# Kernel tuning notes

Measured on AMD Instinct MI355X. Metric: run time of the kernel, lower is better.

The kernel has to match this reference:

```python
import jax, jax.numpy as jnp
import numpy as np

V, WD, H, B, S, A = 50000, 300, 300, 64, 128, 8
H2 = 2 * H
NEG = -1e9


def _reverse_padded(x, lens):
    # reverse each sequence within its valid length; zeros elsewhere
    T = x.shape[1]
    idx = lens[:, None] - 1 - jnp.arange(T)[None, :]          # [B,T]
    valid = (idx >= 0)
    idx = jnp.clip(idx, 0, T - 1)
    return jnp.take_along_axis(x, idx[:, :, None], axis=1) * valid[:, :, None]


def _lstm_dir(x, lens, Wih, Whh, bih, bhh):
    # single-direction LSTM; emulates pack_padded: state frozen and output 0 past lens
    Bn, T, _ = x.shape
    Hn = Whh.shape[1]
    h0 = jnp.zeros((Bn, Hn), x.dtype)
    valid = (jnp.arange(T)[None, :] < lens[:, None]).astype(x.dtype)  # [B,T]

    def step(carry, inp):
        h, c = carry
        xt, vt = inp                                          # xt [B,D], vt [B,1]
        g = xt @ Wih.T + bih + h @ Whh.T + bhh                # [B,4H]
        i, f, gg, o = jnp.split(g, 4, axis=-1)                # torch gate order i,f,g,o
        i = jax.nn.sigmoid(i); f = jax.nn.sigmoid(f)
        o = jax.nn.sigmoid(o); gg = jnp.tanh(gg)
        c_new = f * c + i * gg
        h_new = o * jnp.tanh(c_new)
        h = vt * h_new + (1.0 - vt) * h
        c = vt * c_new + (1.0 - vt) * c
        return (h, c), vt * h_new

    _, outs = jax.lax.scan(step, (h0, h0), (x.transpose(1, 0, 2), valid.T[:, :, None]))
    return outs.transpose(1, 0, 2)                            # [B,T,H]


def _bilstm(x, lens, Wih, Whh, bih, bhh):
    fwd = _lstm_dir(x, lens, Wih[0], Whh[0], bih[0], bhh[0])
    xr = _reverse_padded(x, lens)
    bwd = _lstm_dir(xr, lens, Wih[1], Whh[1], bih[1], bhh[1])
    bwd = _reverse_padded(bwd, lens)
    return jnp.concatenate([fwd, bwd], axis=-1)               # [B,T,2H]


def setup_inputs() -> dict:
    key = jax.random.key(0)
    ks = jax.random.split(key, 16)
    lens_t = jax.random.randint(ks[0], (B,), S // 2, S + 1)
    ids_t = jax.random.randint(ks[1], (B, S), 1, V)
    text = jnp.where(jnp.arange(S)[None, :] < lens_t[:, None], ids_t, 0)
    lens_a = jax.random.randint(ks[2], (B,), 2, A + 1)
    ids_a = jax.random.randint(ks[3], (B, A), 1, V)
    aspect_ids = jnp.where(jnp.arange(A)[None, :] < lens_a[:, None], ids_a, 0)
    position_weight = jax.random.uniform(ks[4], (B, S), jnp.float32) * (text != 0)
    s = 0.05
    emb = jax.random.normal(ks[5], (V, WD), jnp.float32) * s
    emb = emb.at[0].set(0.0)  # padding row

    def lstm_params(k):
        k1, k2, k3, k4 = jax.random.split(k, 4)
        return (jax.random.normal(k1, (2, 4 * H, WD), jnp.float32) * s,
                jax.random.normal(k2, (2, 4 * H, H), jnp.float32) * s,
                jax.random.normal(k3, (2, 4 * H), jnp.float32) * s,
                jax.random.normal(k4, (2, 4 * H), jnp.float32) * s)

    l1_Wih, l1_Whh, l1_bih, l1_bhh = lstm_params(ks[6])
    l2_Wih, l2_Whh, l2_bih, l2_bhh = lstm_params(ks[7])
    return dict(
        text=text, aspect_ids=aspect_ids, position_weight=position_weight, emb=emb,
        l1_Wih=l1_Wih, l1_Whh=l1_Whh, l1_bih=l1_bih, l1_bhh=l1_bhh,
        l2_Wih=l2_Wih, l2_Whh=l2_Whh, l2_bih=l2_bih, l2_bhh=l2_bhh,
        lin1_W=jax.random.normal(ks[8], (2, H2, 2 * H2), jnp.float32) * s,
        lin1_b=jax.random.normal(ks[9], (2, H2), jnp.float32) * s,
        lin2_W=jax.random.normal(ks[10], (2, 1, H2), jnp.float32) * s,
        lin2_b=jax.random.normal(ks[11], (2, 1), jnp.float32) * s,
        fc_W=jax.random.normal(ks[12], (3, H2), jnp.float32) * s,
        fc_b=jax.random.normal(ks[13], (3,), jnp.float32) * s,
    )


def reference(text, aspect_ids, position_weight, emb,
              l1_Wih, l1_Whh, l1_bih, l1_bhh,
              l2_Wih, l2_Whh, l2_bih, l2_bhh,
              lin1_W, lin1_b, lin2_W, lin2_b, fc_W, fc_b):
    text_len = jnp.sum(text != 0, axis=-1)
    asp_len = jnp.sum(aspect_ids != 0, axis=-1)
    masks = (text != 0).astype(jnp.float32)          # [B,S]
    tmasks = (aspect_ids != 0).astype(jnp.float32)   # [B,A]
    wf = emb[text]                                    # [B,S,WD]
    af = emb[aspect_ids]                              # [B,A,WD]
    v = _bilstm(wf, text_len, l1_Wih, l1_Whh, l1_bih, l1_bhh)   # [B,S,2H]
    e = _bilstm(af, asp_len, l2_Wih, l2_Whh, l2_bih, l2_bhh)    # [B,A,2H]
    pair_mask = masks[:, :, None] * tmasks[:, None, :]          # [B,S,A]
    for i in range(2):
        a = jnp.einsum('bsd,bad->bsa', v, e)
        a = jnp.where(pair_mask == 0, NEG, a)
        a = jax.nn.softmax(a, axis=2)
        mid = jnp.einsum('bsa,bad->bsd', a, e)                  # [B,S,2H]
        mid = jnp.concatenate([mid, v], axis=-1)                # [B,S,4H]
        mid = jax.nn.leaky_relu(mid @ lin1_W[i].T + lin1_b[i])  # [B,S,2H]
        t = jax.nn.sigmoid(v @ lin2_W[i].T + lin2_b[i])         # [B,S,1]
        v = (1.0 - t) * mid + t * v
        v = position_weight[:, :, None] * v
    e_masked = jnp.where(tmasks[:, :, None] == 0, NEG, e)
    query = jnp.max(e_masked, axis=1)                           # [B,2H]
    alpha = jnp.einsum('bsd,bd->bs', v, query)
    alpha = jnp.where(masks == 0, NEG, alpha)
    alpha = jax.nn.softmax(alpha, axis=1)
    z = jnp.einsum('bs,bsd->bd', alpha, v)                      # [B,2H]
    return z @ fc_W.T + fc_b                                    # [B,3]
```

## Files before the change

### kernel.cpp

```cpp
#include <hip/hip_runtime.h>
#include <hip/hip_bf16.h>
#include <hip/hip_fp16.h>


typedef unsigned short u16;
typedef __attribute__((ext_vector_type(8))) short short8;
typedef __attribute__((ext_vector_type(4))) float floatx4;

#define NEGV -1e9f
#define MFMA __builtin_amdgcn_mfma_f32_16x16x32_bf16

__device__ __forceinline__ float bf2f(u16 u) {
    union { unsigned int i; float f; } x; x.i = ((unsigned int)u) << 16; return x.f;
}
__device__ __forceinline__ u16 f2bf(float f) {
    unsigned int u = __float_as_uint(f);
    unsigned int r = (u + 0x7fff + ((u >> 16) & 1)) >> 16;
    return (u16)r;
}
__device__ __forceinline__ float h16(u16 u) {
    __half h; *(u16*)&h = u; return __half2float(h);
}
__device__ __forceinline__ u16 f16(float f) {
    __half h = __float2half(f); return *(u16*)&h;
}
__device__ __forceinline__ float sigm(float x) { return 1.f / (1.f + expf(-x)); }
__device__ __forceinline__ float rdf(const void* p, size_t i, int flag) {
    return flag ? ((const float*)p)[i] : bf2f(((const u16*)p)[i]);
}

#if defined(__has_builtin)
# if __has_builtin(__builtin_amdgcn_fdot2)
#  define USE_FDOT2_BUILTIN 1
# endif
#endif
typedef __attribute__((ext_vector_type(2))) _Float16 half2v;
__device__ __forceinline__ float dot2f(unsigned int w, unsigned int h, float acc) {
#ifdef USE_FDOT2_BUILTIN
    union { unsigned int u; half2v v; } a, b;
    a.u = w; b.u = h;
    return __builtin_amdgcn_fdot2(a.v, b.v, acc, false);
#else
    asm("v_dot2_f32_f16 %0, %1, %2, %0" : "+v"(acc) : "v"(w), "v"(h));
    return acc;
#endif
}

__global__ void k_detect(const void* __restrict__ emb, int* __restrict__ flag) {
    __shared__ int cnt;
    if (threadIdx.x == 0) cnt = 0;
    __syncthreads();
    u16 x = ((const u16*)emb)[4096 + threadIdx.x];
    int e = (x >> 7) & 0xFF;
    if (e >= 0x8A) atomicAdd(&cnt, 1);
    __syncthreads();
    if (threadIdx.x == 0) *flag = (cnt > 8) ? 1 : 0;
}

__global__ void k_prep_small(const int* __restrict__ text, const int* __restrict__ asp,
                             int* __restrict__ lens) {
    int tid = threadIdx.x;
    if (tid < 64) {
        int c = 0;
        for (int s = 0; s < 128; ++s) c += (text[tid * 128 + s] != 0);
        lens[tid] = c;
    } else if (tid < 128) {
        int b = tid - 64; int c = 0;
        for (int a = 0; a < 8; ++a) c += (asp[b * 8 + a] != 0);
        lens[64 + b] = c;
    }
}

__global__ void k_pad_wih2(const void* __restrict__ W1, const void* __restrict__ W2,
                           const int* __restrict__ flag,
                           u16* __restrict__ d1h, u16* __restrict__ d1l,
                           u16* __restrict__ d2h, u16* __restrict__ d2l) {
    int i = blockIdx.x * 256 + threadIdx.x;
    if (i >= 2 * 2432 * 320) return;
    int f = *flag;
    int layer = i / (2432 * 320), r = i - layer * (2432 * 320);
    int n = r / 320, k = r - n * 320;
    const void* W = layer ? W2 : W1;
    float val = (n < 2400 && k < 300) ? rdf(W, (size_t)n * 300 + k, f) : 0.f;
    u16 hi = f2bf(val);
    float lo = val - bf2f(hi);
    if (layer) { d2h[r] = hi; d2l[r] = f2bf(lo); }
    else       { d1h[r] = hi; d1l[r] = f2bf(lo); }
}

__global__ void k_whhT2(const void* __restrict__ W1, const void* __restrict__ W2,
                        const int* __restrict__ flag,
                        u16* __restrict__ d1, u16* __restrict__ d2) {
    int i = blockIdx.x * 256 + threadIdx.x;
    if (i >= 2 * 720000) return;
    int f = *flag;
    int layer = i / 720000, r = i - layer * 720000;
    int dir = r / 360000, rr = r - dir * 360000;
    int kp = rr / 2400, t = rr - kp * 2400;
    int cc = t >> 1, j = t & 1;
    int k = 2 * kp + j;
    const void* W = layer ? W2 : W1;
    u16 bits = f16(rdf(W, (size_t)dir * 360000 + (size_t)cc * 300 + k, f));
    if (layer) d2[r] = bits; else d1[r] = bits;
}

__global__ void k_pad_lin1AB(const void* __restrict__ W, const int* __restrict__ flag,
                             u16* __restrict__ Ahi, u16* __restrict__ Alo,
                             u16* __restrict__ Bhi, u16* __restrict__ Blo) {
    int i = blockIdx.x * 256 + threadIdx.x;
    if (i >= 2 * 640 * 608) return;
    int f = *flag;
    int it = i / (640 * 608), r = i - it * (640 * 608);
    int n = r / 608, k = r - n * 608;
    float va = 0.f, vb = 0.f;
    if (n < 600 && k < 600) {
        va = rdf(W, (size_t)it * 720000 + (size_t)n * 1200 + k, f);
        vb = rdf(W, (size_t)it * 720000 + (size_t)n * 1200 + 600 + k, f);
    }
    u16 h;
    h = f2bf(va); Ahi[i] = h; Alo[i] = f2bf(va - bf2f(h));
    h = f2bf(vb); Bhi[i] = h; Blo[i] = f2bf(vb - bf2f(h));
}

__global__ void k_esplit(const float* __restrict__ e,
                         u16* __restrict__ ehi, u16* __restrict__ elo) {
    int i = blockIdx.x * 256 + threadIdx.x;
    if (i >= 512 * 608) return;
    int r = i / 608, k = i - r * 608;
    float val = (k < 600) ? e[r * 600 + k] : 0.f;
    u16 h = f2bf(val);
    ehi[i] = h;
    elo[i] = f2bf(val - bf2f(h));
}

__global__ void k_small(const void* pw, const void* l2w, const void* l2b,
                        const void* fcw, const void* fcb, const void* lb,
                        const void* b1i, const void* b1h, const void* b2i, const void* b2h,
                        const int* __restrict__ flag,
                        float* __restrict__ dst, float* __restrict__ bl,
                        float* __restrict__ bt, float* __restrict__ ba) {
    int i = blockIdx.x * 256 + threadIdx.x;
    int f = *flag;
    if (i < 8192)            dst[i] = rdf(pw, i, f);
    else if (i < 9392)       dst[i] = rdf(l2w, i - 8192, f);
    else if (i < 9394)       dst[i] = rdf(l2b, i - 9392, f);
    else if (i < 11194)      dst[i] = rdf(fcw, i - 9394, f);
    else if (i < 11197)      dst[i] = rdf(fcb, i - 11194, f);
    if (i < 1280) {
        int dir = i / 640, c = i - dir * 640;
        bl[i] = (c < 600) ? rdf(lb, dir * 600 + c, f) : 0.f;
    }
    if (i < 2400) {
        bt[i] = rdf(b1i, i, f) + rdf(b1h, i, f);
        ba[i] = rdf(b2i, i, f) + rdf(b2h, i, f);
    }
}

__device__ __forceinline__ void gemm_emb_tile(
    const void* __restrict__ emb, const int* __restrict__ ids,
    int base, int rpb, int stride, int f,
    const u16* __restrict__ Bhi, const u16* __restrict__ Blo,
    const float* __restrict__ bias,
    u16* __restrict__ C, int ldc, int nstore, int bx, int by, int tid)
{
    int wave = tid >> 6, lane = tid & 63;
    int l15 = lane & 15, quad = lane >> 4;
    int m0 = bx * 64 + wave * 16;
    int n0 = by * 64;

    int m = m0 + l15;
    int b = m / rpb, j = m - b * rpb;
    int id = ids[b * stride + base + j];
    const float* arow_f = (const float*)emb + (size_t)id * 300;
    const u16*   arow_b = (const u16*)emb + (size_t)id * 300;

    const u16* Bp  = Bhi + (size_t)(n0 + l15) * 320 + quad * 8;
    const u16* Bp2 = Blo + (size_t)(n0 + l15) * 320 + quad * 8;

    floatx4 acc0 = {0.f, 0.f, 0.f, 0.f};
    floatx4 acc1 = acc0, acc2 = acc0, acc3 = acc0;

    for (int kc = 0; kc < 10; ++kc) {
        int ko = kc * 32 + quad * 8;
        short8 ahi, alo;
        if (f) {
            if (ko + 8 <= 300) {
                float4 fa = *(const float4*)(arow_f + ko);
                float4 fb = *(const float4*)(arow_f + ko + 4);
                float vv[8] = {fa.x, fa.y, fa.z, fa.w, fb.x, fb.y, fb.z, fb.w};
                #pragma unroll
                for (int t = 0; t < 8; ++t) {
                    u16 h = f2bf(vv[t]);
                    ahi[t] = (short)h;
                    alo[t] = (short)f2bf(vv[t] - bf2f(h));
                }
            } else {
                #pragma unroll
                for (int t = 0; t < 8; ++t) {
                    int k = ko + t;
                    float vv = (k < 300) ? arow_f[k] : 0.f;
                    u16 h = f2bf(vv);
                    ahi[t] = (short)h;
                    alo[t] = (short)f2bf(vv - bf2f(h));
                }
            }
        } else {
            #pragma unroll
            for (int t = 0; t < 8; ++t) {
                int k = ko + t;
                ahi[t] = (k < 300) ? (short)arow_b[k] : (short)0;
                alo[t] = 0;
            }
        }
        int ko2 = kc * 32;
        short8 bh0 = *(const short8*)(Bp + ko2);
        short8 bh1 = *(const short8*)(Bp + (size_t)16 * 320 + ko2);
        short8 bh2 = *(const short8*)(Bp + (size_t)32 * 320 + ko2);
        short8 bh3 = *(const short8*)(Bp + (size_t)48 * 320 + ko2);
        short8 bl0 = *(const short8*)(Bp2 + ko2);
        short8 bl1 = *(const short8*)(Bp2 + (size_t)16 * 320 + ko2);
        short8 bl2 = *(const short8*)(Bp2 + (size_t)32 * 320 + ko2);
        short8 bl3 = *(const short8*)(Bp2 + (size_t)48 * 320 + ko2);
        acc0 = MFMA(ahi, bh0, acc0, 0, 0, 0);
        acc1 = MFMA(ahi, bh1, acc1, 0, 0, 0);
        acc2 = MFMA(ahi, bh2, acc2, 0, 0, 0);
        acc3 = MFMA(ahi, bh3, acc3, 0, 0, 0);
        acc0 = MFMA(ahi, bl0, acc0, 0, 0, 0);
        acc1 = MFMA(ahi, bl1, acc1, 0, 0, 0);
        acc2 = MFMA(ahi, bl2, acc2, 0, 0, 0);
        acc3 = MFMA(ahi, bl3, acc3, 0, 0, 0);
        acc0 = MFMA(alo, bh0, acc0, 0, 0, 0);
        acc1 = MFMA(alo, bh1, acc1, 0, 0, 0);
        acc2 = MFMA(alo, bh2, acc2, 0, 0, 0);
        acc3 = MFMA(alo, bh3, acc3, 0, 0, 0);
    }

    #pragma unroll
    for (int c = 0; c < 4; ++c) {
        floatx4 acc = (c == 0) ? acc0 : (c == 1) ? acc1 : (c == 2) ? acc2 : acc3;
        int col = n0 + c * 16 + l15;
        if (col >= nstore) continue;
        float bb = bias[col];
        #pragma unroll
        for (int r = 0; r < 4; ++r) {
            int row = m0 + quad * 4 + r;
            C[(size_t)row * ldc + col] = f16(acc[r] + bb);
        }
    }
}

__global__ __launch_bounds__(256) void gemm_embk(
    const void* __restrict__ emb, const int* __restrict__ ids,
    int base, int rpb, int stride, const int* __restrict__ flag,
    const u16* __restrict__ Bhi, const u16* __restrict__ Blo,
    const float* __restrict__ bias,
    u16* __restrict__ C, int ldc, int nstore)
{
    gemm_emb_tile(emb, ids, base, rpb, stride, *flag, Bhi, Blo, bias,
                  C, ldc, nstore, blockIdx.x, blockIdx.y, threadIdx.x);
}

__device__ __forceinline__ void gemm_core(
    const u16* __restrict__ Ap, const u16* __restrict__ Ap2,
    const u16* __restrict__ Bp, const u16* __restrict__ Bp2,
    int lda, int ldb, int nk,
    floatx4& acc0, floatx4& acc1, floatx4& acc2, floatx4& acc3)
{
    for (int kc = 0; kc < nk; ++kc) {
        int ko = kc * 32;
        short8 bh0 = *(const short8*)(Bp + ko);
        short8 bh1 = *(const short8*)(Bp + (size_t)16 * ldb + ko);
        short8 bh2 = *(const short8*)(Bp + (size_t)32 * ldb + ko);
        short8 bh3 = *(const short8*)(Bp + (size_t)48 * ldb + ko);
        short8 bl0 = *(const short8*)(Bp2 + ko);
        short8 bl1 = *(const short8*)(Bp2 + (size_t)16 * ldb + ko);
        short8 bl2 = *(const short8*)(Bp2 + (size_t)32 * ldb + ko);
        short8 bl3 = *(const short8*)(Bp2 + (size_t)48 * ldb + ko);
        short8 a  = *(const short8*)(Ap + ko);
        short8 al = *(const short8*)(Ap2 + ko);
        acc0 = MFMA(a, bh0, acc0, 0, 0, 0);
        acc1 = MFMA(a, bh1, acc1, 0, 0, 0);
        acc2 = MFMA(a, bh2, acc2, 0, 0, 0);
        acc3 = MFMA(a, bh3, acc3, 0, 0, 0);
        acc0 = MFMA(a, bl0, acc0, 0, 0, 0);
        acc1 = MFMA(a, bl1, acc1, 0, 0, 0);
        acc2 = MFMA(a, bl2, acc2, 0, 0, 0);
        acc3 = MFMA(a, bl3, acc3, 0, 0, 0);
        acc0 = MFMA(al, bh0, acc0, 0, 0, 0);
        acc1 = MFMA(al, bh1, acc1, 0, 0, 0);
        acc2 = MFMA(al, bh2, acc2, 0, 0, 0);
        acc3 = MFMA(al, bh3, acc3, 0, 0, 0);
    }
}

__global__ __launch_bounds__(256) void gemm_ew(
    const u16* __restrict__ Ahi, const u16* __restrict__ Alo,
    const u16* __restrict__ l1a_hi, const u16* __restrict__ l1a_lo,
    float* __restrict__ EW)
{
    int tid = threadIdx.x;
    int wave = tid >> 6, lane = tid & 63;
    int l15 = lane & 15, quad = lane >> 4;
    int iter = blockIdx.z;
    int m0 = blockIdx.x * 64 + wave * 16;
    int n0 = blockIdx.y * 64;
    const u16* Ap  = Ahi + (size_t)(m0 + l15) * 608 + quad * 8;
    const u16* Ap2 = Alo + (size_t)(m0 + l15) * 608 + quad * 8;
    const u16* Bp  = l1a_hi + (size_t)iter * 640 * 608 + (size_t)(n0 + l15) * 608 + quad * 8;
    const u16* Bp2 = l1a_lo + (size_t)iter * 640 * 608 + (size_t)(n0 + l15) * 608 + quad * 8;
    floatx4 acc0 = {0.f, 0.f, 0.f, 0.f};
    floatx4 acc1 = acc0, acc2 = acc0, acc3 = acc0;
    gemm_core(Ap, Ap2, Bp, Bp2, 608, 608, 19, acc0, acc1, acc2, acc3);
    #pragma unroll
    for (int c = 0; c < 4; ++c) {
        floatx4 acc = (c == 0) ? acc0 : (c == 1) ? acc1 : (c == 2) ? acc2 : acc3;
        int col = n0 + c * 16 + l15;
        if (col >= 600) continue;
        #pragma unroll
        for (int r = 0; r < 4; ++r) {
            int row = m0 + quad * 4 + r;
            EW[((size_t)iter * 512 + row) * 600 + col] = acc[r];
        }
    }
}

__global__ __launch_bounds__(256) void gemm_vt(
    const u16* __restrict__ vhi, const u16* __restrict__ vlo,
    const u16* __restrict__ Bhi, const u16* __restrict__ Blo,
    const float* __restrict__ bias,
    const float* __restrict__ EW, const float* __restrict__ a_sm,
    const float* __restrict__ tg, const float* __restrict__ pw,
    float* __restrict__ vio)
{
    __shared__ float al_s[64][8];
    __shared__ float ew_s[8][64];
    int tid = threadIdx.x;
    int wave = tid >> 6, lane = tid & 63;
    int l15 = lane & 15, quad = lane >> 4;
    int m0 = blockIdx.x * 64 + wave * 16;
    int n0 = blockIdx.y * 64;
    int row0 = blockIdx.x * 64;
    int bidx = row0 >> 7;

    for (int i = tid; i < 512; i += 256)
        al_s[i >> 3][i & 7] = a_sm[(size_t)(row0 + (i >> 3)) * 8 + (i & 7)];
    for (int i = tid; i < 512; i += 256) {
        int a = i >> 6, cc = i & 63;
        int col = n0 + cc;
        ew_s[a][cc] = (col < 600) ? EW[((size_t)bidx * 8 + a) * 600 + col] : 0.f;
    }
    __syncthreads();

    const u16* Ap  = vhi + (size_t)(m0 + l15) * 608 + quad * 8;
    const u16* Ap2 = vlo + (size_t)(m0 + l15) * 608 + quad * 8;
    const u16* Bp  = Bhi + (size_t)(n0 + l15) * 608 + quad * 8;
    const u16* Bp2 = Blo + (size_t)(n0 + l15) * 608 + quad * 8;
    floatx4 acc0 = {0.f, 0.f, 0.f, 0.f};
    floatx4 acc1 = acc0, acc2 = acc0, acc3 = acc0;
    gemm_core(Ap, Ap2, Bp, Bp2, 608, 608, 19, acc0, acc1, acc2, acc3);

    #pragma unroll
    for (int c = 0; c < 4; ++c) {
        floatx4 acc = (c == 0) ? acc0 : (c == 1) ? acc1 : (c == 2) ? acc2 : acc3;
        int cc = c * 16 + l15;
        int col = n0 + cc;
        if (col >= 600) continue;
        float bb = bias[col];
        #pragma unroll
        for (int r = 0; r < 4; ++r) {
            int rr = wave * 16 + quad * 4 + r;
            int row = row0 + rr;
            float mid = 0.f;
            #pragma unroll
            for (int a = 0; a < 8; ++a) mid += al_s[rr][a] * ew_s[a][cc];
            float val = acc[r] + bb + mid;
            val = val > 0.f ? val : 0.01f * val;
            float t = tg[row];
            size_t vi = (size_t)row * 600 + col;
            float vv = vio[vi];
            vio[vi] = pw[row] * ((1.f - t) * val + t * vv);
        }
    }
}

__global__ __launch_bounds__(960, 1) void k_lstm6(
    const u16* __restrict__ xf, const u16* __restrict__ xb, int ldx, int rpb,
    int base_f, int base_b, const u16* __restrict__ whhT,
    const int* __restrict__ lens, float* __restrict__ out, int T, int init,
    float* __restrict__ hst, float* __restrict__ cst, int nsteps,
    const u16* __restrict__ xa, const u16* __restrict__ whhA,
    const int* __restrict__ lensA, float* __restrict__ outA,
    float* __restrict__ hstA, float* __restrict__ cstA, int nLstm,
    const void* __restrict__ emb, const int* __restrict__ text,
    int bf_next, int bb_next, const int* __restrict__ flag,
    const u16* __restrict__ wih_hi, const u16* __restrict__ wih_lo,
    const float* __restrict__ bias_t,
    u16* __restrict__ xf_next, u16* __restrict__ xb_next)
{
    __shared__ float part2[6][2][600];
    __shared__ u16 wlds[6][4][2][1200];
    __shared__ __align__(4) u16 hs16[304];
    int blk = blockIdx.x;
    if (blk >= nLstm) {
        if (threadIdx.x >= 256) return;
        int g = blk - nLstm;
        int dirn = g / 608; int t = g - dirn * 608;
        int bx = t & 31, by = t >> 5;
        gemm_emb_tile(emb, text, dirn ? bb_next : bf_next, 32, 128, *flag,
                      wih_hi + (dirn ? 1200ull * 320 : 0),
                      wih_lo + (dirn ? 1200ull * 320 : 0),
                      bias_t + (dirn ? 1200 : 0),
                      dirn ? xb_next : xf_next, 1200, 1200, bx, by, threadIdx.x);
        return;
    }
    if (blk >= 128) {
        blk -= 128;
        xf = xa; xb = xa + 1200; ldx = 2400; rpb = 8;
        base_f = 0; base_b = 0;
        whhT = whhA; lens = lensA; out = outA; T = 8; init = 1;
        hst = hstA; cst = cstA; nsteps = 8;
    }
    int tid = threadIdx.x;
    int g6 = tid / 160, u = tid - g6 * 160;
    bool act = (u < 150);
    int b = blk >> 1, dir = blk & 1;
    int len = lens[b];
    float c = 0.f, hf = 0.f;
    const u16* wbase = whhT + (size_t)dir * 360000 + (size_t)g6 * 60000 + 16 * u;

    uint4 wA[8], wB[8];
    if (act) {
        #pragma unroll
        for (int r = 0; r < 8; ++r) {
            wA[r] = *(const uint4*)(wbase + (size_t)r * 2400);
            wB[r] = *(const uint4*)(wbase + (size_t)r * 2400 + 8);
        }
        #pragma unroll
        for (int r = 0; r < 4; ++r) {
            *(uint4*)&wlds[g6][r][0][8 * u] = *(const uint4*)(wbase + (size_t)(8 + r) * 2400);
            *(uint4*)&wlds[g6][r][1][8 * u] = *(const uint4*)(wbase + (size_t)(8 + r) * 2400 + 8);
        }
    } else {
        #pragma unroll
        for (int r = 0; r < 8; ++r) {
            wA[r] = uint4{0u, 0u, 0u, 0u};
            wB[r] = uint4{0u, 0u, 0u, 0u};
        }
    }
    #pragma unroll
    for (int r = 0; r < 8; ++r) {
        asm volatile("" : "+v"(wA[r].x), "+v"(wA[r].y), "+v"(wA[r].z), "+v"(wA[r].w));
        asm volatile("" : "+v"(wB[r].x), "+v"(wB[r].y), "+v"(wB[r].z), "+v"(wB[r].w));
    }
    if (tid < 300) {
        hf = init ? 0.f : hst[(size_t)blk * 300 + tid];
        c  = init ? 0.f : cst[(size_t)blk * 300 + tid];
        hs16[tid] = f16(hf);
    }
    __syncthreads();
    const u16* wstream = wbase + (size_t)12 * 2400;

    for (int s = 0; s < nsteps; ++s) {
        int pos = dir ? (base_b + nsteps - 1 - s) : (base_f + s);
        if (pos >= len) continue;
        if (act) {
            float a0 = 0.f, a1 = 0.f, a2 = 0.f, a3 = 0.f;
            float a4 = 0.f, a5 = 0.f, a6 = 0.f, a7 = 0.f;
            const unsigned int* h2p = (const unsigned int*)(hs16 + g6 * 50);
            #define DOT8(va, vb, hh)                                   \
                a0 = dot2f((va).x, hh, a0); a1 = dot2f((va).y, hh, a1);\
                a2 = dot2f((va).z, hh, a2); a3 = dot2f((va).w, hh, a3);\
                a4 = dot2f((vb).x, hh, a4); a5 = dot2f((vb).y, hh, a5);\
                a6 = dot2f((vb).z, hh, a6); a7 = dot2f((vb).w, hh, a7);
            #pragma unroll
            for (int r = 0; r < 8; ++r) {
                unsigned int h2 = h2p[r];
                DOT8(wA[r], wB[r], h2);
            }
            #pragma unroll
            for (int r = 0; r < 4; ++r) {
                unsigned int h2 = h2p[8 + r];
                uint4 va = *(const uint4*)&wlds[g6][r][0][8 * u];
                uint4 vb = *(const uint4*)&wlds[g6][r][1][8 * u];
                DOT8(va, vb, h2);
            }
            const u16* wp = wstream;
            #pragma unroll 4
            for (int i = 0; i < 13; ++i) {
                unsigned int h2 = h2p[12 + i];
                uint4 va = *(const uint4*)wp;
                uint4 vb = *(const uint4*)(wp + 8);
                wp += 2400;
                DOT8(va, vb, h2);
            }
            #undef DOT8
            float4 w0 = {a0, a1, a2, a3};
            float4 w1 = {a4, a5, a6, a7};
            *(float4*)&part2[g6][0][4 * u] = w0;
            *(float4*)&part2[g6][1][4 * u] = w1;
        }
        __syncthreads();
        if (tid < 300) {
            const u16* xr = dir ? (xb + (size_t)(b * rpb + pos - base_b) * ldx)
                                : (xf + (size_t)(b * rpb + pos - base_f) * ldx);
            float gi = h16(xr[tid]), gf = h16(xr[300 + tid]);
            float gg = h16(xr[600 + tid]), go = h16(xr[900 + tid]);
            #pragma unroll
            for (int g = 0; g < 6; ++g) {
                int c0 = tid,       i0 = ((c0 >> 3) << 2) | (c0 & 3);
                int c1 = 300 + tid, i1 = ((c1 >> 3) << 2) | (c1 & 3);
                int c2 = 600 + tid, i2 = ((c2 >> 3) << 2) | (c2 & 3);
                int c3 = 900 + tid, i3 = ((c3 >> 3) << 2) | (c3 & 3);
                gi += part2[g][(c0 >> 2) & 1][i0];
                gf += part2[g][(c1 >> 2) & 1][i1];
                gg += part2[g][(c2 >> 2) & 1][i2];
                go += part2[g][(c3 >> 2) & 1][i3];
            }
            gi = sigm(gi); gf = sigm(gf); gg = tanhf(gg); go = sigm(go);
            c = gf * c + gi * gg;
            float hn = go * tanhf(c);
            out[((size_t)b * T + pos) * 600 + dir * 300 + tid] = hn;
            hf = hn;
            hs16[tid] = f16(hn);
        }
        __syncthreads();
    }
    if (tid < 300) {
        hst[(size_t)blk * 300 + tid] = hf;
        cst[(size_t)blk * 300 + tid] = c;
    }
}

__global__ __launch_bounds__(128) void k_scorev(
    const float* __restrict__ v, const float* __restrict__ e,
    const int* __restrict__ text, const int* __restrict__ asp,
    const float* __restrict__ l2w, const float* __restrict__ l2b, int iter,
    float* __restrict__ a_sm, float* __restrict__ tg,
    u16* __restrict__ vhi, u16* __restrict__ vlo)
{
    __shared__ float vs[600];
    __shared__ float red[2][9];
    int row = blockIdx.x;
    int b = row >> 7;
    int t = threadIdx.x, wv = t >> 6, lane = t & 63;
    const float* vrow = v + (size_t)row * 600;
    const float* eb = e + (size_t)b * 4800;
    const float* w2 = l2w + iter * 600;

    for (int d = t; d < 600; d += 128) vs[d] = vrow[d];
    __syncthreads();

    float acc[9];
    #pragma unroll
    for (int j = 0; j < 9; ++j) acc[j] = 0.f;
    for (int d = t; d < 600; d += 128) {
        float vv = vs[d];
        #pragma unroll
        for (int a = 0; a < 8; ++a) acc[a] += vv * eb[a * 600 + d];
        acc[8] += vv * w2[d];
    }
    #pragma unroll
    for (int off = 32; off >= 1; off >>= 1) {
        #pragma unroll
        for (int j = 0; j < 9; ++j) acc[j] += __shfl_down(acc[j], off, 64);
    }
    if (lane == 0) {
        #pragma unroll
        for (int j = 0; j < 9; ++j) red[wv][j] = acc[j];
    }
    __syncthreads();
    if (t == 0) {
        float dots[9];
        #pragma unroll
        for (int j = 0; j < 9; ++j) dots[j] = red[0][j] + red[1][j];
        tg[row] = sigm(dots[8] + l2b[iter]);
        bool sm = (text[row] != 0);
        float sc[8]; float mx = -INFINITY;
        #pragma unroll
        for (int a = 0; a < 8; ++a) {
            sc[a] = (sm && asp[b * 8 + a] != 0) ? dots[a] : NEGV;
            mx = fmaxf(mx, sc[a]);
        }
        float den = 0.f;
        #pragma unroll
        for (int a = 0; a < 8; ++a) { sc[a] = expf(sc[a] - mx); den += sc[a]; }
        float inv = 1.f / den;
        #pragma unroll
        for (int a = 0; a < 8; ++a) a_sm[(size_t)row * 8 + a] = sc[a] * inv;
    }
    for (int d = t; d < 608; d += 128) {
        float val = (d < 600) ? vs[d] : 0.f;
        u16 h = f2bf(val);
        vhi[(size_t)row * 608 + d] = h;
        vlo[(size_t)row * 608 + d] = f2bf(val - bf2f(h));
    }
}

__global__ void k_query(const float* __restrict__ e, const int* __restrict__ asp,
                        float* __restrict__ q) {
    int i = blockIdx.x * 256 + threadIdx.x;
    if (i >= 64 * 600) return;
    int b = i / 600, d = i - b * 600;
    float m = NEGV;
    for (int a = 0; a < 8; ++a)
        if (asp[b * 8 + a] != 0) m = fmaxf(m, e[(size_t)b * 4800 + a * 600 + d]);
    q[i] = m;
}

__global__ __launch_bounds__(128) void k_final(
    const float* __restrict__ v, const float* __restrict__ q,
    const int* __restrict__ text, const float* __restrict__ fcW,
    const float* __restrict__ fcb, const int* __restrict__ flag, void* __restrict__ outv)
{
    __shared__ float red[128];
    __shared__ float al[128];
    __shared__ float zz[600];
    int b = blockIdx.x, s = threadIdx.x;
    const float* vrow = v + (size_t)(b * 128 + s) * 600;
    const float* qb = q + (size_t)b * 600;
    float sc = 0.f;
    for (int d = 0; d < 600; ++d) sc += vrow[d] * qb[d];
    if (text[b * 128 + s] == 0) sc = NEGV;
    red[s] = sc; __syncthreads();
    for (int off = 64; off >= 1; off >>= 1) {
        if (s < off) red[s] = fmaxf(red[s], red[s + off]);
        __syncthreads();
    }
    float mx = red[0]; __syncthreads();
    float ex = expf(sc - mx);
    red[s] = ex; __syncthreads();
    for (int off = 64; off >= 1; off >>= 1) {
        if (s < off) red[s] += red[s + off];
        __syncthreads();
    }
    float alpha = ex / red[0];
    al[s] = alpha; __syncthreads();
    for (int d = s; d < 600; d += 128) {
        float z = 0.f;
        for (int s2 = 0; s2 < 128; ++s2) z += al[s2] * v[(size_t)(b * 128 + s2) * 600 + d];
        zz[d] = z;
    }
    __syncthreads();
    if (s < 3) {
        float o = 0.f;
        for (int d = 0; d < 600; ++d) o += zz[d] * fcW[s * 600 + d];
        o += fcb[s];
        if (*flag) ((float*)outv)[b * 3 + s] = o;
        else       ((u16*)outv)[b * 3 + s] = f2bf(o);
    }
}

extern "C" void kernel_launch(void* const* d_in, const int* in_sizes, int n_in,
                              void* d_out, int out_size, void* d_ws, size_t ws_size,
                              hipStream_t stream) {
    const int*  text   = (const int*)d_in[0];
    const int*  asp    = (const int*)d_in[1];
    const void* pw     = d_in[2];
    const void* emb    = d_in[3];
    const void* l1_Wih = d_in[4];
    const void* l1_Whh = d_in[5];
    const void* l1_bih = d_in[6];
    const void* l1_bhh = d_in[7];
    const void* l2_Wih = d_in[8];
    const void* l2_Whh = d_in[9];
    const void* l2_bih = d_in[10];
    const void* l2_bhh = d_in[11];
    const void* lin1_W = d_in[12];
    const void* lin1_b = d_in[13];
    const void* lin2_W = d_in[14];
    const void* lin2_b = d_in[15];
    const void* fcW    = d_in[16];
    const void* fcb    = d_in[17];
    (void)ws_size; (void)n_in; (void)in_sizes; (void)out_size;

    char* w = (char*)d_ws;
    size_t off = 0;
    auto alloc = [&](size_t bytes) -> void* {
        void* p = w + off;
        off += (bytes + 255) & ~(size_t)255;
        return p;
    };
    int*   flag     = (int*)  alloc(4);
    int*   lens     = (int*)  alloc(128ull * 4);
    float* bias_t   = (float*)alloc(2400ull * 4);
    float* bias_a   = (float*)alloc(2400ull * 4);
    float* bias_l1  = (float*)alloc(1280ull * 4);
    float* smallf   = (float*)alloc(11197ull * 4);
    float* tg       = (float*)alloc(8192ull * 4);
    float* a_sm     = (float*)alloc(8192ull * 8 * 4);
    float* query    = (float*)alloc(64ull * 600 * 4);
    float* hst_t    = (float*)alloc(128ull * 300 * 4);
    float* cst_t    = (float*)alloc(128ull * 300 * 4);
    float* hst_a    = (float*)alloc(128ull * 300 * 4);
    float* cst_a    = (float*)alloc(128ull * 300 * 4);
    float* e        = (float*)alloc(512ull * 600 * 4);
    float* v        = (float*)alloc(8192ull * 600 * 4);
    float* pw_f     = smallf;
    float* l2w_f    = smallf + 8192;
    float* l2b_f    = smallf + 9392;
    float* fcW_f    = smallf + 9394;
    float* fcb_f    = smallf + 11194;
    size_t phase_off = off;
    u16*   wiht_hi  = (u16*)  alloc(2432ull * 320 * 2);
    u16*   wiht_lo  = (u16*)  alloc(2432ull * 320 * 2);
    u16*   wiha_hi  = (u16*)  alloc(2432ull * 320 * 2);
    u16*   wiha_lo  = (u16*)  alloc(2432ull * 320 * 2);
    u16*   whhT_t   = (u16*)  alloc(720000ull * 2);
    u16*   whhT_a   = (u16*)  alloc(720000ull * 2);
    u16*   xf0      = (u16*)  alloc(2048ull * 1200 * 2);
    u16*   xb0      = (u16*)  alloc(2048ull * 1200 * 2);
    u16*   xf1      = (u16*)  alloc(2048ull * 1200 * 2);
    u16*   xb1      = (u16*)  alloc(2048ull * 1200 * 2);
    u16*   xproj_a  = (u16*)  alloc(512ull * 2400 * 2);
    off = phase_off;
    u16*   l1a_hi   = (u16*)  alloc(2ull * 640 * 608 * 2);
    u16*   l1a_lo   = (u16*)  alloc(2ull * 640 * 608 * 2);
    u16*   l1b_hi   = (u16*)  alloc(2ull * 640 * 608 * 2);
    u16*   l1b_lo   = (u16*)  alloc(2ull * 640 * 608 * 2);
    u16*   ehi      = (u16*)  alloc(512ull * 608 * 2);
    u16*   elo      = (u16*)  alloc(512ull * 608 * 2);
    float* EW       = (float*)alloc(2ull * 512 * 600 * 4);
    u16*   vhi      = (u16*)  alloc(8192ull * 608 * 2);
    u16*   vlo      = (u16*)  alloc(8192ull * 608 * 2);

    hipMemsetAsync(v, 0, 8192ull * 600 * 4, stream);
    hipMemsetAsync(e, 0, 512ull * 600 * 4, stream);

    k_detect<<<1, 256, 0, stream>>>(emb, flag);
    k_prep_small<<<1, 128, 0, stream>>>(text, asp, lens);
    k_pad_wih2<<<(2 * 2432 * 320 + 255) / 256, 256, 0, stream>>>(
        l1_Wih, l2_Wih, flag, wiht_hi, wiht_lo, wiha_hi, wiha_lo);
    k_whhT2<<<(2 * 720000 + 255) / 256, 256, 0, stream>>>(
        l1_Whh, l2_Whh, flag, whhT_t, whhT_a);
    k_small<<<49, 256, 0, stream>>>(pw, lin2_W, lin2_b, fcW, fcb, lin1_b,
                                    l1_bih, l1_bhh, l2_bih, l2_bhh, flag,
                                    smallf, bias_l1, bias_t, bias_a);

    gemm_embk<<<dim3(8, 38), 256, 0, stream>>>(emb, asp, 0, 8, 8, flag,
        wiha_hi, wiha_lo, bias_a, xproj_a, 2400, 2400);
    gemm_embk<<<dim3(32, 19), 256, 0, stream>>>(emb, text, 0, 32, 128, flag,
        wiht_hi, wiht_lo, bias_t, xf0, 1200, 1200);
    gemm_embk<<<dim3(32, 19), 256, 0, stream>>>(emb, text, 96, 32, 128, flag,
        wiht_hi + 1200ull * 320, wiht_lo + 1200ull * 320, bias_t + 1200,
        xb0, 1200, 1200);

    for (int kk = 0; kk < 4; ++kk) {
        int bf = 32 * kk;
        int bb = 96 - 32 * kk;
        u16* xfc = (kk & 1) ? xf1 : xf0;
        u16* xbc = (kk & 1) ? xb1 : xb0;
        u16* xfn = (kk & 1) ? xf0 : xf1;
        u16* xbn = (kk & 1) ? xb0 : xb1;
        int nLstm = (kk == 0) ? 256 : 128;
        int haveNext = (kk < 3);
        int nblk = nLstm + (haveNext ? 1216 : 0);
        k_lstm6<<<nblk, 960, 0, stream>>>(xfc, xbc, 1200, 32, bf, bb,
            whhT_t, lens, v, 128, kk == 0 ? 1 : 0, hst_t, cst_t, 32,
            xproj_a, whhT_a, lens + 64, e, hst_a, cst_a, nLstm,
            emb, text, bf + 32, bb - 32, flag, wiht_hi, wiht_lo, bias_t,
            xfn, xbn);
    }

    k_pad_lin1AB<<<(2 * 640 * 608 + 255) / 256, 256, 0, stream>>>(
        lin1_W, flag, l1a_hi, l1a_lo, l1b_hi, l1b_lo);
    k_esplit<<<(512 * 608 + 255) / 256, 256, 0, stream>>>(e, ehi, elo);
    gemm_ew<<<dim3(8, 10, 2), 256, 0, stream>>>(ehi, elo, l1a_hi, l1a_lo, EW);

    for (int iter = 0; iter < 2; ++iter) {
        k_scorev<<<8192, 128, 0, stream>>>(v, e, text, asp, l2w_f, l2b_f,
            iter, a_sm, tg, vhi, vlo);
        gemm_vt<<<dim3(128, 10), 256, 0, stream>>>(vhi, vlo,
            l1b_hi + (size_t)iter * 640 * 608, l1b_lo + (size_t)iter * 640 * 608,
            bias_l1 + iter * 640, EW + (size_t)iter * 512 * 600,
            a_sm, tg, pw_f, v);
    }

    k_query<<<150, 256, 0, stream>>>(e, asp, query);
    k_final<<<64, 128, 0, stream>>>(v, query, text, fcW_f, fcb_f, flag, d_out);
}
```

Measured before the change: 1.116 ms.

## Split each LSTM recurrence across two blocks exchanging partial gates via global memory

Each LSTM chain (batch, direction) is now split across a pair of workgroups, each owning half of the hidden units (150), so the kernel launches twice as many recurrent blocks. Each block computes partial gate pre-activations for all 1200 gates from its half of h, publishes the peer's half through a global exchange buffer, and spins on a per-block step counter flag for the peer's contribution. This spreads the serial recurrence over more CUs and drops the register-resident weights, but adds a cross-block global-memory handshake on every timestep. It also relies on both blocks of a pair being co-resident, which is a deadlock risk.

```diff
diff --git a/kernel.cpp b/kernel.cpp
--- a/kernel.cpp
+++ b/kernel.cpp
@@ -390,20 +390,21 @@
     float* __restrict__ hst, float* __restrict__ cst, int nsteps,
     const u16* __restrict__ xa, const u16* __restrict__ whhA,
     const int* __restrict__ lensA, float* __restrict__ outA,
-    float* __restrict__ hstA, float* __restrict__ cstA, int nLstm,
+    float* __restrict__ hstA, float* __restrict__ cstA, int nSplit,
     const void* __restrict__ emb, const int* __restrict__ text,
     int bf_next, int bb_next, const int* __restrict__ flag,
     const u16* __restrict__ wih_hi, const u16* __restrict__ wih_lo,
     const float* __restrict__ bias_t,
-    u16* __restrict__ xf_next, u16* __restrict__ xb_next)
+    u16* __restrict__ xf_next, u16* __restrict__ xb_next,
+    float* __restrict__ exch, unsigned int* __restrict__ flags)
 {
-    __shared__ float part2[6][2][600];
-    __shared__ u16 wlds[6][4][2][1200];
-    __shared__ __align__(4) u16 hs16[304];
+    __shared__ float part2[5][2][600];
+    __shared__ u16 wlds[5][2][2][1200];
+    __shared__ __align__(4) u16 hs16[152];
     int blk = blockIdx.x;
-    if (blk >= nLstm) {
+    if (blk >= nSplit) {
         if (threadIdx.x >= 256) return;
-        int g = blk - nLstm;
+        int g = blk - nSplit;
         int dirn = g / 608; int t = g - dirn * 608;
         int bx = t & 31, by = t >> 5;
         gemm_emb_tile(emb, text, dirn ? bb_next : bf_next, 32, 128, *flag,
@@ -413,81 +414,97 @@
                       dirn ? xb_next : xf_next, 1200, 1200, bx, by, threadIdx.x);
         return;
     }
-    if (blk >= 128) {
-        blk -= 128;
+    int me = blk, peer = blk ^ 1;
+    int kseg = blk & 1;
+    int chain = blk >> 1;
+    if (chain >= 128) {
+        chain -= 128;
         xf = xa; xb = xa + 1200; ldx = 2400; rpb = 8;
         base_f = 0; base_b = 0;
         whhT = whhA; lens = lensA; out = outA; T = 8; init = 1;
         hst = hstA; cst = cstA; nsteps = 8;
     }
     int tid = threadIdx.x;
-    int g6 = tid / 160, u = tid - g6 * 160;
+    int g6 = tid / 192, u = tid - g6 * 192;
     bool act = (u < 150);
-    int b = blk >> 1, dir = blk & 1;
+    int b = chain >> 1, dir = chain & 1;
     int len = lens[b];
     float c = 0.f, hf = 0.f;
-    const u16* wbase = whhT + (size_t)dir * 360000 + (size_t)g6 * 60000 + 16 * u;
-
-    uint4 wA[8], wB[8];
+    const u16* wbase = whhT + (size_t)dir * 360000
+                     + (size_t)(kseg * 75 + g6 * 15) * 2400 + 16 * u;
     if (act) {
         #pragma unroll
-        for (int r = 0; r < 8; ++r) {
-            wA[r] = *(const uint4*)(wbase + (size_t)r * 2400);
-            wB[r] = *(const uint4*)(wbase + (size_t)r * 2400 + 8);
-        }
-        #pragma unroll
-        for (int r = 0; r < 4; ++r) {
-            *(uint4*)&wlds[g6][r][0][8 * u] = *(const uint4*)(wbase + (size_t)(8 + r) * 2400);
-            *(uint4*)&wlds[g6][r][1][8 * u] = *(const uint4*)(wbase + (size_t)(8 + r) * 2400 + 8);
-        }
-    } else {
-        #pragma unroll
-        for (int r = 0; r < 8; ++r) {
-            wA[r] = uint4{0u, 0u, 0u, 0u};
-            wB[r] = uint4{0u, 0u, 0u, 0u};
-        }
-    }
+        for (int r = 0; r < 2; ++r) {
+            *(uint4*)&wlds[g6][r][0][8 * u] = *(const uint4*)(wbase + (size_t)r * 2400);
+            *(uint4*)&wlds[g6][r][1][8 * u] = *(const uint4*)(wbase + (size_t)r * 2400 + 8);
+        }
+    }
+    int e_abs = kseg * 150 + tid;
+    if (tid < 150) {
+        hf = init ? 0.f : hst[(size_t)chain * 300 + e_abs];
+        c  = init ? 0.f : cst[(size_t)chain * 300 + e_abs];
+        hs16[tid] = f16(hf);
+    }
+    int gH[4], gI[4];
     #pragma unroll
-    for (int r = 0; r < 8; ++r) {
-        asm volatile("" : "+v"(wA[r].x), "+v"(wA[r].y), "+v"(wA[r].z), "+v"(wA[r].w));
-        asm volatile("" : "+v"(wB[r].x), "+v"(wB[r].y), "+v"(wB[r].z), "+v"(wB[r].w));
-    }
-    if (tid < 300) {
-        hf = init ? 0.f : hst[(size_t)blk * 300 + tid];
-        c  = init ? 0.f : cst[(size_t)blk * 300 + tid];
-        hs16[tid] = f16(hf);
+    for (int k = 0; k < 4; ++k) {
+        int ck = e_abs + 300 * k;
+        gH[k] = (ck >> 2) & 1;
+        gI[k] = ((ck >> 3) << 2) | (ck & 3);
+    }
+    int pH = 0, pI = 0;
+    if (tid < 600) {
+        int r = tid % 150, q = tid / 150;
+        int pc = (kseg ^ 1) * 150 + r + 300 * q;
+        pH = (pc >> 2) & 1;
+        pI = ((pc >> 3) << 2) | (pc & 3);
+    }
+    float* exme = exch + (size_t)me * 1200;
+    const float* expe = exch + (size_t)peer * 1200;
+    unsigned int* flg_me = flags + me * 16;
+    unsigned int* flg_pe = flags + peer * 16;
+    unsigned int cnt = 0;
+    if (!init) {
+        if (dir == 0) {
+            int e0 = len < base_f ? len : base_f;
+            cnt = (unsigned)e0;
+        } else {
+            int kk = base_f >> 5;
+            for (int j = 0; j < kk; ++j) {
+                int e0 = len - (96 - 32 * j);
+                e0 = e0 < 0 ? 0 : (e0 > 32 ? 32 : e0);
+                cnt += (unsigned)e0;
+            }
+        }
     }
     __syncthreads();
-    const u16* wstream = wbase + (size_t)12 * 2400;
+    const u16* wstream = wbase + (size_t)2 * 2400;
+    const unsigned int* h2p = (const unsigned int*)hs16 + g6 * 15;
 
     for (int s = 0; s < nsteps; ++s) {
         int pos = dir ? (base_b + nsteps - 1 - s) : (base_f + s);
         if (pos >= len) continue;
+        ++cnt;
+        int par = (int)(cnt & 1u);
         if (act) {
             float a0 = 0.f, a1 = 0.f, a2 = 0.f, a3 = 0.f;
             float a4 = 0.f, a5 = 0.f, a6 = 0.f, a7 = 0.f;
-            const unsigned int* h2p = (const unsigned int*)(hs16 + g6 * 50);
             #define DOT8(va, vb, hh)                                   \
                 a0 = dot2f((va).x, hh, a0); a1 = dot2f((va).y, hh, a1);\
                 a2 = dot2f((va).z, hh, a2); a3 = dot2f((va).w, hh, a3);\
                 a4 = dot2f((vb).x, hh, a4); a5 = dot2f((vb).y, hh, a5);\
                 a6 = dot2f((vb).z, hh, a6); a7 = dot2f((vb).w, hh, a7);
             #pragma unroll
-            for (int r = 0; r < 8; ++r) {
+            for (int r = 0; r < 2; ++r) {
                 unsigned int h2 = h2p[r];
-                DOT8(wA[r], wB[r], h2);
-            }
-            #pragma unroll
-            for (int r = 0; r < 4; ++r) {
-                unsigned int h2 = h2p[8 + r];
                 uint4 va = *(const uint4*)&wlds[g6][r][0][8 * u];
                 uint4 vb = *(const uint4*)&wlds[g6][r][1][8 * u];
                 DOT8(va, vb, h2);
             }
             const u16* wp = wstream;
-            #pragma unroll 4
+            #pragma unroll 13
             for (int i = 0; i < 13; ++i) {
-                unsigned int h2 = h2p[12 + i];
+                unsigned int h2 = h2p[2 + i];
                 uint4 va = *(const uint4*)wp;
                 uint4 vb = *(const uint4*)(wp + 8);
                 wp += 2400;
@@ -500,34 +517,61 @@
             *(float4*)&part2[g6][1][4 * u] = w1;
         }
         __syncthreads();
-        if (tid < 300) {
+        if (tid < 600) {
+            float s5 = part2[0][pH][pI] + part2[1][pH][pI] + part2[2][pH][pI]
+                     + part2[3][pH][pI] + part2[4][pH][pI];
+            __hip_atomic_store(exme + par * 600 + tid, s5,
+                               __ATOMIC_RELAXED, __HIP_MEMORY_SCOPE_AGENT);
+        }
+        asm volatile("s_waitcnt vmcnt(0)" ::: "memory");
+        __syncthreads();
+        if (tid == 0) {
+            __hip_atomic_store(flg_me, cnt, __ATOMIC_RELEASE,
+                               __HIP_MEMORY_SCOPE_AGENT);
+            while (__hip_atomic_load(flg_pe, __ATOMIC_ACQUIRE,
+                                     __HIP_MEMORY_SCOPE_AGENT) < cnt)
+                __builtin_amdgcn_s_sleep(2);
+        }
+        __syncthreads();
+        if (tid < 150) {
             const u16* xr = dir ? (xb + (size_t)(b * rpb + pos - base_b) * ldx)
                                 : (xf + (size_t)(b * rpb + pos - base_f) * ldx);
-            float gi = h16(xr[tid]), gf = h16(xr[300 + tid]);
-            float gg = h16(xr[600 + tid]), go = h16(xr[900 + tid]);
-            #pragma unroll
-            for (int g = 0; g < 6; ++g) {
-                int c0 = tid,       i0 = ((c0 >> 3) << 2) | (c0 & 3);
-                int c1 = 300 + tid, i1 = ((c1 >> 3) << 2) | (c1 & 3);
-                int c2 = 600 + tid, i2 = ((c2 >> 3) << 2) | (c2 & 3);
-                int c3 = 900 + tid, i3 = ((c3 >> 3) << 2) | (c3 & 3);
-                gi += part2[g][(c0 >> 2) & 1][i0];
-                gf += part2[g][(c1 >> 2) & 1][i1];
-                gg += part2[g][(c2 >> 2) & 1][i2];
-                go += part2[g][(c3 >> 2) & 1][i3];
-            }
+            float p0 = part2[0][gH[0]][gI[0]] + part2[1][gH[0]][gI[0]]
+                     + part2[2][gH[0]][gI[0]] + part2[3][gH[0]][gI[0]]
+                     + part2[4][gH[0]][gI[0]];
+            float p1 = part2[0][gH[1]][gI[1]] + part2[1][gH[1]][gI[1]]
+                     + part2[2][gH[1]][gI[1]] + part2[3][gH[1]][gI[1]]
+                     + part2[4][gH[1]][gI[1]];
+            float p2 = part2[0][gH[2]][gI[2]] + part2[1][gH[2]][gI[2]]
+                     + part2[2][gH[2]][gI[2]] + part2[3][gH[2]][gI[2]]
+                     + part2[4][gH[2]][gI[2]];
+            float p3 = part2[0][gH[3]][gI[3]] + part2[1][gH[3]][gI[3]]
+                     + part2[2][gH[3]][gI[3]] + part2[3][gH[3]][gI[3]]
+                     + part2[4][gH[3]][gI[3]];
+            float q0 = __hip_atomic_load(expe + par * 600 + tid,
+                                         __ATOMIC_RELAXED, __HIP_MEMORY_SCOPE_AGENT);
+            float q1 = __hip_atomic_load(expe + par * 600 + 150 + tid,
+                                         __ATOMIC_RELAXED, __HIP_MEMORY_SCOPE_AGENT);
+            float q2 = __hip_atomic_load(expe + par * 600 + 300 + tid,
+                                         __ATOMIC_RELAXED, __HIP_MEMORY_SCOPE_AGENT);
+            float q3 = __hip_atomic_load(expe + par * 600 + 450 + tid,
+                                         __ATOMIC_RELAXED, __HIP_MEMORY_SCOPE_AGENT);
+            float gi = h16(xr[e_abs])       + p0 + q0;
+            float gf = h16(xr[300 + e_abs]) + p1 + q1;
+            float gg = h16(xr[600 + e_abs]) + p2 + q2;
+            float go = h16(xr[900 + e_abs]) + p3 + q3;
             gi = sigm(gi); gf = sigm(gf); gg = tanhf(gg); go = sigm(go);
             c = gf * c + gi * gg;
             float hn = go * tanhf(c);
-            out[((size_t)b * T + pos) * 600 + dir * 300 + tid] = hn;
+            out[((size_t)b * T + pos) * 600 + dir * 300 + e_abs] = hn;
             hf = hn;
             hs16[tid] = f16(hn);
         }
         __syncthreads();
     }
-    if (tid < 300) {
-        hst[(size_t)blk * 300 + tid] = hf;
-        cst[(size_t)blk * 300 + tid] = c;
+    if (tid < 150) {
+        hst[(size_t)chain * 300 + e_abs] = hf;
+        cst[(size_t)chain * 300 + e_abs] = c;
     }
 }
 
@@ -695,6 +739,8 @@
     float* cst_a    = (float*)alloc(128ull * 300 * 4);
     float* e        = (float*)alloc(512ull * 600 * 4);
     float* v        = (float*)alloc(8192ull * 600 * 4);
+    float* exch     = (float*)alloc(512ull * 1200 * 4);
+    unsigned int* lflags = (unsigned int*)alloc(512ull * 16 * 4);
     float* pw_f     = smallf;
     float* l2w_f    = smallf + 8192;
     float* l2b_f    = smallf + 9392;
@@ -725,6 +771,7 @@
 
     hipMemsetAsync(v, 0, 8192ull * 600 * 4, stream);
     hipMemsetAsync(e, 0, 512ull * 600 * 4, stream);
+    hipMemsetAsync(lflags, 0, 512ull * 16 * 4, stream);
 
     k_detect<<<1, 256, 0, stream>>>(emb, flag);
     k_prep_small<<<1, 128, 0, stream>>>(text, asp, lens);
@@ -751,14 +798,14 @@
         u16* xbc = (kk & 1) ? xb1 : xb0;
         u16* xfn = (kk & 1) ? xf0 : xf1;
         u16* xbn = (kk & 1) ? xb0 : xb1;
-        int nLstm = (kk == 0) ? 256 : 128;
+        int nSplit = (kk == 0) ? 512 : 256;
         int haveNext = (kk < 3);
-        int nblk = nLstm + (haveNext ? 1216 : 0);
+        int nblk = nSplit + (haveNext ? 1216 : 0);
         k_lstm6<<<nblk, 960, 0, stream>>>(xfc, xbc, 1200, 32, bf, bb,
             whhT_t, lens, v, 128, kk == 0 ? 1 : 0, hst_t, cst_t, 32,
-            xproj_a, whhT_a, lens + 64, e, hst_a, cst_a, nLstm,
+            xproj_a, whhT_a, lens + 64, e, hst_a, cst_a, nSplit,
             emb, text, bf + 32, bb - 32, flag, wiht_hi, wiht_lo, bias_t,
-            xfn, xbn);
+            xfn, xbn, exch, lflags);
     }
 
     k_pad_lin1AB<<<(2 * 640 * 608 + 255) / 256, 256, 0, stream>>>(
```

Result: slower. 2.075 ms (+85.9%).
